# Optimization experiments

Hardware: AMD Instinct MI355X
Metric: run time of the kernel (lower is better)

The kernel has to match this reference:

```python
import jax, jax.numpy as jnp
import numpy as np

NUM_HEADS = 4
OUTPUT_DIM = 64


def setup_inputs() -> dict:
    key = jax.random.key(0)
    k1, k2, k3 = jax.random.split(key, 3)
    B, N, F = 8, 2048, 256
    features = jax.random.normal(k1, (B, N, F), dtype=jnp.float32)
    adj_matrix = jax.random.uniform(k2, (B, N, N), dtype=jnp.float32)
    # learned params (glorot-ish scale)
    kernel = jax.random.normal(k3, (F, OUTPUT_DIM * NUM_HEADS), dtype=jnp.float32) * (1.0 / np.sqrt(F))
    bias = jnp.zeros((OUTPUT_DIM * NUM_HEADS,), dtype=jnp.float32)
    return {"features": features, "adj_matrix": adj_matrix, "kernel": kernel, "bias": bias}


def reference(features, adj_matrix, kernel, bias):
    B, N, F = features.shape
    H, D = NUM_HEADS, OUTPUT_DIM
    Wh = jnp.matmul(features, kernel)                 # [B, N, H*D]
    Whh = Wh.reshape(B, N, H, D)                      # [B, N, H, D]
    # per-node, per-head score: inner product Wh1 @ Wh2 = ||Wh||^2
    e = jnp.sum(Whh * Whh, axis=-1)                   # [B, N, H]
    attention = jax.nn.softmax(e, axis=1)             # softmax over nodes
    attention = jnp.mean(attention, axis=2)           # head mean -> [B, N]
    # adjacency mask (broadcast column score over neighbors)
    A = attention[:, :, None] * adj_matrix            # [B, N, N]
    out = jnp.matmul(A, Wh) + bias                    # [B, N, H*D]
    return jax.nn.relu(out)
```

## Files before the change

### kernel.cpp

```cpp
#include <hip/hip_runtime.h>
#include <hip/hip_bf16.h>

#define BATCH 8
#define NNODE 2048
#define FDIM 256
#define HD 256
#define NH 4
#define MROWS (BATCH*NNODE)

typedef float f32x4 __attribute__((ext_vector_type(4)));
typedef short s16x8 __attribute__((ext_vector_type(8)));
typedef unsigned short ushort_t;

#define MFMA __builtin_amdgcn_mfma_f32_16x16x32_bf16
#define SCHED0() __builtin_amdgcn_sched_barrier(0)
#define SBAR() __builtin_amdgcn_s_barrier()

__device__ __forceinline__ void split2(float f, ushort_t& h, ushort_t& l) {
    unsigned u = __builtin_bit_cast(unsigned, f);
    h = (ushort_t)(u >> 16);
    float fh = __builtin_bit_cast(float, u & 0xffff0000u);
    float lo = f - fh;
    l = (ushort_t)(__builtin_bit_cast(unsigned, lo) >> 16);
}

#define GLOAD16(gp, lp) __builtin_amdgcn_global_load_lds( \
    (const __attribute__((address_space(1))) void*)(gp),  \
    (__attribute__((address_space(3))) void*)(lp), 16, 0, 0)

__global__ __launch_bounds__(256) void wprep_kernel(
    const float* __restrict__ Wm,
    ushort_t* __restrict__ wt_hi, ushort_t* __restrict__ wt_lo)
{
    const int nn = blockIdx.x, k = threadIdx.x;
    ushort_t h, l;
    split2(Wm[(size_t)k * HD + nn], h, l);
    wt_hi[nn * FDIM + k] = h;
    wt_lo[nn * FDIM + k] = l;
}

__global__ __launch_bounds__(256, 4) void gemm1_kernel(
    const float* __restrict__ features,
    const ushort_t* __restrict__ wt_hi,
    const ushort_t* __restrict__ wt_lo,
    ushort_t* __restrict__ WhT_hi,
    ushort_t* __restrict__ WhT_lo,
    float* __restrict__ e_out)
{
    __shared__ __align__(16) ushort_t Ah[64 * 64];
    __shared__ __align__(16) ushort_t Al[64 * 64];
    __shared__ __align__(16) ushort_t Bh[64 * 64];
    __shared__ __align__(16) ushort_t Bl[64 * 64];
    __shared__ float red[64][2];

    const int tid = threadIdx.x, lane = tid & 63, w = tid >> 6;
    const int wr = w >> 1, wc = w & 1;
    const int row0 = blockIdx.x * 64;
    const int head = blockIdx.y;
    const int col0 = head * 64;

    const float* Ab = features + (size_t)row0 * FDIM;
    const ushort_t* Bhg = wt_hi + (size_t)col0 * FDIM;
    const ushort_t* Blg = wt_lo + (size_t)col0 * FDIM;

    const int sr0 = tid >> 3;
    const int sg8 = tid & 7;
    const int bc = (lane >> 3);
    const int bs = lane & 7;

    f32x4 ar[4];
    f32x4 acc[2][2];
    #pragma unroll
    for (int m = 0; m < 2; ++m)
        #pragma unroll
        for (int n = 0; n < 2; ++n) acc[m][n] = (f32x4)0.f;

    #define G1_LOADA(K0) do {                                                  \
        _Pragma("unroll")                                                      \
        for (int i = 0; i < 2; ++i) {                                          \
            const int r = sr0 + 32 * i;                                        \
            ar[2*i]   = *(const f32x4*)&Ab[(size_t)r * FDIM + (K0) + sg8 * 8]; \
            ar[2*i+1] = *(const f32x4*)&Ab[(size_t)r * FDIM + (K0) + sg8 * 8 + 4]; \
        }                                                                      \
    } while (0)

    #define G1_STAGEA() do {                                                   \
        _Pragma("unroll")                                                      \
        for (int i = 0; i < 2; ++i) {                                          \
            const int r = sr0 + 32 * i;                                        \
            s16x8 vh, vl; ushort_t hh, ll;                                     \
            _Pragma("unroll")                                                  \
            for (int j = 0; j < 4; ++j) {                                      \
                split2(ar[2*i][j], hh, ll);  vh[j] = (short)hh; vl[j] = (short)ll; \
            }                                                                  \
            _Pragma("unroll")                                                  \
            for (int j = 0; j < 4; ++j) {                                      \
                split2(ar[2*i+1][j], hh, ll); vh[4+j] = (short)hh; vl[4+j] = (short)ll; \
            }                                                                  \
            const int off = r * 64 + ((sg8 ^ (r & 7)) << 3);                   \
            *(s16x8*)&Ah[off] = vh; *(s16x8*)&Al[off] = vl;                    \
        }                                                                      \
    } while (0)

    #define G1_STAGEB(K0) do {                                                 \
        _Pragma("unroll")                                                      \
        for (int qq = 0; qq < 2; ++qq) {                                       \
            const int q = w + qq * 4;                                          \
            const int c = q * 8 + bc;                                          \
            const int g = bs ^ (c & 7);                                        \
            GLOAD16(&Bhg[(size_t)c * FDIM + (K0) + g * 8], &Bh[q * 512]);      \
            GLOAD16(&Blg[(size_t)c * FDIM + (K0) + g * 8], &Bl[q * 512]);      \
        }                                                                      \
    } while (0)

    G1_LOADA(0);
    for (int t = 0; t < 4; ++t) {
        G1_STAGEB(t * 64);
        G1_STAGEA();
        if (t < 3) G1_LOADA((t + 1) * 64);
        if (t < 3) { asm volatile("s_waitcnt lgkmcnt(0) vmcnt(4)" ::: "memory"); }
        else       { asm volatile("s_waitcnt lgkmcnt(0) vmcnt(0)" ::: "memory"); }
        SCHED0(); SBAR(); SCHED0();
        #pragma unroll
        for (int kh = 0; kh < 2; ++kh) {
            const int kg = kh * 4 + (lane >> 4);
            s16x8 afh[2], afl[2], bfh[2], bfl[2];
            #pragma unroll
            for (int m = 0; m < 2; ++m) {
                const int r = wr * 32 + m * 16 + (lane & 15);
                const int off = r * 64 + ((kg ^ (r & 7)) << 3);
                afh[m] = *(const s16x8*)&Ah[off];
                afl[m] = *(const s16x8*)&Al[off];
            }
            #pragma unroll
            for (int n = 0; n < 2; ++n) {
                const int c = wc * 32 + n * 16 + (lane & 15);
                const int off = c * 64 + ((kg ^ (c & 7)) << 3);
                bfh[n] = *(const s16x8*)&Bh[off];
                bfl[n] = *(const s16x8*)&Bl[off];
            }
            #pragma unroll
            for (int m = 0; m < 2; ++m)
                #pragma unroll
                for (int n = 0; n < 2; ++n) {
                    acc[m][n] = MFMA(afh[m], bfh[n], acc[m][n], 0, 0, 0);
                    acc[m][n] = MFMA(afh[m], bfl[n], acc[m][n], 0, 0, 0);
                    acc[m][n] = MFMA(afl[m], bfh[n], acc[m][n], 0, 0, 0);
                }
        }
        SCHED0(); SBAR(); SCHED0();
    }

    #pragma unroll
    for (int m = 0; m < 2; ++m)
        #pragma unroll
        for (int j = 0; j < 4; ++j) {
            float p = acc[m][0][j] * acc[m][0][j] + acc[m][1][j] * acc[m][1][j];
            p += __shfl_xor(p, 1, 64);
            p += __shfl_xor(p, 2, 64);
            p += __shfl_xor(p, 4, 64);
            p += __shfl_xor(p, 8, 64);
            if ((lane & 15) == 0)
                red[wr * 32 + m * 16 + (lane >> 4) * 4 + j][wc] = p;
        }

    __syncthreads();
    ushort_t* Th = Ah;
    ushort_t* Tl = Al;
    #pragma unroll
    for (int m = 0; m < 2; ++m)
        #pragma unroll
        for (int n = 0; n < 2; ++n)
            #pragma unroll
            for (int j = 0; j < 4; ++j) {
                const int rr = wr * 32 + m * 16 + (lane >> 4) * 4 + j;
                const int cc = wc * 32 + n * 16 + (lane & 15);
                const int ad = cc * 64 + ((((rr >> 3) ^ (cc & 7))) << 3) + (rr & 7);
                ushort_t hh, ll;
                split2(acc[m][n][j], hh, ll);
                Th[ad] = hh; Tl[ad] = ll;
            }
    __syncthreads();

    if (tid < 64) {
        const int rg = row0 + tid;
        e_out[((size_t)((rg >> 11) * NH + head)) * NNODE + (rg & 2047)] =
            red[tid][0] + red[tid][1];
    }
    const int bb = row0 >> 11, node0 = row0 & 2047;
    #pragma unroll
    for (int i = 0; i < 2; ++i) {
        const int gid = tid + 256 * i;
        const int c = gid >> 3, gr = gid & 7;
        const int ad = c * 64 + ((gr ^ (c & 7)) << 3);
        uint4 vh = *(const uint4*)&Th[ad];
        uint4 vl = *(const uint4*)&Tl[ad];
        const size_t o = ((size_t)bb * HD + col0 + c) * NNODE + node0 + gr * 8;
        *(uint4*)&WhT_hi[o] = vh;
        *(uint4*)&WhT_lo[o] = vl;
    }
}

__global__ __launch_bounds__(256) void sm_kernel(
    const float* __restrict__ e, float* __restrict__ ms)
{
    __shared__ float red[8];
    const int bh = blockIdx.x, tid = threadIdx.x;
    const int lane = tid & 63, w = tid >> 6;
    const float* row = e + (size_t)bh * NNODE;
    float mx = -3.0e38f;
    for (int n = tid; n < NNODE; n += 256) mx = fmaxf(mx, row[n]);
    #pragma unroll
    for (int off = 32; off; off >>= 1) mx = fmaxf(mx, __shfl_xor(mx, off, 64));
    if (lane == 0) red[w] = mx;
    __syncthreads();
    mx = fmaxf(fmaxf(red[0], red[1]), fmaxf(red[2], red[3]));
    float s = 0.f;
    for (int n = tid; n < NNODE; n += 256) s += expf(row[n] - mx);
    #pragma unroll
    for (int off = 32; off; off >>= 1) s += __shfl_xor(s, off, 64);
    if (lane == 0) red[4 + w] = s;
    __syncthreads();
    if (tid == 0) {
        ms[bh * 2] = mx;
        ms[bh * 2 + 1] = red[4] + red[5] + red[6] + red[7];
    }
}

__global__ __launch_bounds__(256) void att_kernel(
    const float* __restrict__ e, const float* __restrict__ ms,
    float* __restrict__ attv)
{
    const int i = blockIdx.x * 256 + threadIdx.x;
    const int b = i >> 11, n = i & 2047;
    float a = 0.f;
    #pragma unroll
    for (int h = 0; h < NH; ++h) {
        const int bh = b * NH + h;
        a += expf(e[(size_t)bh * NNODE + n] - ms[bh * 2]) / ms[bh * 2 + 1];
    }
    attv[i] = 0.25f * a;
}

__global__ __launch_bounds__(256, 2) void gemm2_kernel(
    const float* __restrict__ adj,
    const ushort_t* __restrict__ WhT_hi,
    const ushort_t* __restrict__ WhT_lo,
    const float* __restrict__ att,
    const float* __restrict__ bias,
    float* __restrict__ out)
{
    __shared__ __align__(16) ushort_t Bh[3][64 * 64];
    __shared__ __align__(16) ushort_t Bl[3][64 * 64];

    const int tid = threadIdx.x, lane = tid & 63, w = tid >> 6;
    const int b = blockIdx.z;
    const int row0 = blockIdx.x * 128, col0 = blockIdx.y * 64;

    const ushort_t* Bhg = WhT_hi + ((size_t)b * HD + col0) * NNODE;
    const ushort_t* Blg = WhT_lo + ((size_t)b * HD + col0) * NNODE;

    const float* pA = adj + (size_t)b * NNODE * NNODE
                    + (size_t)(row0 + w * 32 + (lane & 15)) * NNODE
                    + ((lane >> 4) * 8);

    const int bc = lane >> 3, bs = lane & 7;

    f32x4 ar[2][2][2];
    s16x8 afh[2][2], afl[2][2];
    f32x4 acc[2][4];
    #pragma unroll
    for (int m = 0; m < 2; ++m)
        #pragma unroll
        for (int n = 0; n < 4; ++n) acc[m][n] = (f32x4)0.f;

    #define G2_LOADA(K0) do {                                                   \
        _Pragma("unroll")                                                       \
        for (int m = 0; m < 2; ++m)                                             \
        _Pragma("unroll")                                                       \
        for (int ks = 0; ks < 2; ++ks) {                                        \
            ar[m][ks][0] = *(const f32x4*)&pA[(size_t)m * 16 * NNODE + (K0) + ks * 32]; \
            ar[m][ks][1] = *(const f32x4*)&pA[(size_t)m * 16 * NNODE + (K0) + ks * 32 + 4]; \
        }                                                                       \
    } while (0)

    #define G2_CONVERT() do {                                                   \
        _Pragma("unroll")                                                       \
        for (int m = 0; m < 2; ++m)                                             \
        _Pragma("unroll")                                                       \
        for (int ks = 0; ks < 2; ++ks) {                                        \
            ushort_t hh, ll;                                                    \
            _Pragma("unroll")                                                   \
            for (int h2 = 0; h2 < 2; ++h2)                                      \
            _Pragma("unroll")                                                   \
            for (int j = 0; j < 4; ++j) {                                       \
                split2(ar[m][ks][h2][j], hh, ll);                               \
                afh[m][ks][h2 * 4 + j] = (short)hh;                             \
                afl[m][ks][h2 * 4 + j] = (short)ll;                             \
            }                                                                   \
        }                                                                       \
    } while (0)

    #define G2_STAGEB(BUF, K0) do {                                             \
        _Pragma("unroll")                                                       \
        for (int qq = 0; qq < 2; ++qq) {                                        \
            const int q = w + qq * 4;                                           \
            const int c = q * 8 + bc;                                           \
            const int g = bs ^ (c & 7);                                         \
            GLOAD16(&Bhg[(size_t)c * NNODE + (K0) + g * 8], &Bh[BUF][q * 512]); \
            GLOAD16(&Blg[(size_t)c * NNODE + (K0) + g * 8], &Bl[BUF][q * 512]); \
        }                                                                       \
    } while (0)

    #define G2_COMPUTE(BHP, BLP) do {                                           \
        _Pragma("unroll")                                                       \
        for (int ks = 0; ks < 2; ++ks) {                                        \
            const int kg = ks * 4 + (lane >> 4);                                \
            s16x8 bfh[4], bfl[4];                                               \
            _Pragma("unroll")                                                   \
            for (int n = 0; n < 4; ++n) {                                       \
                const int c = n * 16 + (lane & 15);                             \
                const int off = c * 64 + ((kg ^ (c & 7)) << 3);                 \
                bfh[n] = *(const s16x8*)&(BHP)[off];                            \
                bfl[n] = *(const s16x8*)&(BLP)[off];                            \
            }                                                                   \
            __builtin_amdgcn_s_setprio(1);                                      \
            _Pragma("unroll")                                                   \
            for (int m = 0; m < 2; ++m)                                         \
            _Pragma("unroll")                                                   \
            for (int n = 0; n < 4; ++n) {                                       \
                acc[m][n] = MFMA(afh[m][ks], bfh[n], acc[m][n], 0, 0, 0);       \
                acc[m][n] = MFMA(afh[m][ks], bfl[n], acc[m][n], 0, 0, 0);       \
                acc[m][n] = MFMA(afl[m][ks], bfh[n], acc[m][n], 0, 0, 0);       \
            }                                                                   \
            __builtin_amdgcn_s_setprio(0);                                      \
        }                                                                       \
    } while (0)

    G2_STAGEB(0, 0);
    G2_LOADA(0);

    int cur = 0;
    for (int t = 0; t < 32; ++t) {
        const int nxt = (cur == 2) ? 0 : cur + 1;
        if (t < 31) G2_STAGEB(nxt, (t + 1) * 64);
        G2_CONVERT();
        if (t < 31) G2_LOADA((t + 1) * 64);
        asm volatile("s_waitcnt vmcnt(12)" ::: "memory");
        SCHED0(); SBAR(); SCHED0();
        {
            const ushort_t* bhp = &Bh[cur][0];
            const ushort_t* blp = &Bl[cur][0];
            G2_COMPUTE(bhp, blp);
        }
        cur = nxt;
    }

    const float* attb = att + (size_t)b * NNODE;
    #pragma unroll
    for (int n = 0; n < 4; ++n) {
        const int c = col0 + n * 16 + (lane & 15);
        const float bv = bias[c];
        #pragma unroll
        for (int m = 0; m < 2; ++m)
            #pragma unroll
            for (int j = 0; j < 4; ++j) {
                const int row = row0 + w * 32 + m * 16 + (lane >> 4) * 4 + j;
                out[((size_t)b * NNODE + row) * HD + c] =
                    fmaxf(fmaf(acc[m][n][j], attb[row], bv), 0.f);
            }
    }
}

extern "C" void kernel_launch(void* const* d_in, const int* in_sizes, int n_in,
                              void* d_out, int out_size, void* d_ws, size_t ws_size,
                              hipStream_t stream) {
    const float* features = (const float*)d_in[0];
    const float* adj      = (const float*)d_in[1];
    const float* Wm       = (const float*)d_in[2];
    const float* bias     = (const float*)d_in[3];
    float* out = (float*)d_out;

    ushort_t* WhT_hi = (ushort_t*)d_ws;
    ushort_t* WhT_lo = WhT_hi + (size_t)BATCH * HD * NNODE;
    ushort_t* wt_hi  = WhT_lo + (size_t)BATCH * HD * NNODE;
    ushort_t* wt_lo  = wt_hi + FDIM * HD;
    float* e    = (float*)(wt_lo + FDIM * HD);
    float* ms   = e + (size_t)BATCH * NH * NNODE;
    float* attv = ms + 64;

    wprep_kernel<<<HD, 256, 0, stream>>>(Wm, wt_hi, wt_lo);
    gemm1_kernel<<<dim3(MROWS / 64, NH), 256, 0, stream>>>(
        features, wt_hi, wt_lo, WhT_hi, WhT_lo, e);
    sm_kernel<<<BATCH * NH, 256, 0, stream>>>(e, ms);
    att_kernel<<<MROWS / 256, 256, 0, stream>>>(e, ms, attv);
    gemm2_kernel<<<dim3(NNODE / 128, HD / 64, BATCH), 256, 0, stream>>>(
        adj, WhT_hi, WhT_lo, attv, bias, out);
}
```

Before: 276.8 us.

## Load B fragments directly from global into registers, dropping LDS staging

The second GEMM no longer stages the bf16 hi/lo WhT tiles through a triple-buffered LDS ring with barriers. Each lane now loads its B fragments straight from global memory into registers, using a manual two-stage register double buffer for A and B-hi, and loads B-lo just in time. This removes LDS traffic and block-wide barriers, but each wave now reads B redundantly from global/L2 and register pressure rises (the occupancy hint of 2 was dropped). It also relies on the compiler's waitcnt placement instead of explicit ones.

Result: slower. 353.2 us (+27.6%).

```diff
diff --git a/kernel.cpp b/kernel.cpp
--- a/kernel.cpp
+++ b/kernel.cpp
@@ -242,7 +242,7 @@
     attv[i] = 0.25f * a;
 }
 
-__global__ __launch_bounds__(256, 2) void gemm2_kernel(
+__global__ __launch_bounds__(256) void gemm2_kernel(
     const float* __restrict__ adj,
     const ushort_t* __restrict__ WhT_hi,
     const ushort_t* __restrict__ WhT_lo,
@@ -250,23 +250,19 @@
     const float* __restrict__ bias,
     float* __restrict__ out)
 {
-    __shared__ __align__(16) ushort_t Bh[3][64 * 64];
-    __shared__ __align__(16) ushort_t Bl[3][64 * 64];
-
     const int tid = threadIdx.x, lane = tid & 63, w = tid >> 6;
     const int b = blockIdx.z;
     const int row0 = blockIdx.x * 128, col0 = blockIdx.y * 64;
 
-    const ushort_t* Bhg = WhT_hi + ((size_t)b * HD + col0) * NNODE;
-    const ushort_t* Blg = WhT_lo + ((size_t)b * HD + col0) * NNODE;
-
     const float* pA = adj + (size_t)b * NNODE * NNODE
                     + (size_t)(row0 + w * 32 + (lane & 15)) * NNODE
                     + ((lane >> 4) * 8);
-
-    const int bc = lane >> 3, bs = lane & 7;
-
-    f32x4 ar[2][2][2];
+    const size_t bbase = ((size_t)b * HD + col0 + (lane & 15)) * NNODE + ((lane >> 4) * 8);
+    const ushort_t* pBh = WhT_hi + bbase;
+    const ushort_t* pBl = WhT_lo + bbase;
+
+    f32x4 a0[8], a1[8];
+    s16x8 bh0[8], bh1[8], bl_[8];
     s16x8 afh[2][2], afl[2][2];
     f32x4 acc[2][4];
     #pragma unroll
@@ -274,17 +270,33 @@
         #pragma unroll
         for (int n = 0; n < 4; ++n) acc[m][n] = (f32x4)0.f;
 
-    #define G2_LOADA(K0) do {                                                   \
+    #define G2_LOADA(AR, K0) do {                                               \
         _Pragma("unroll")                                                       \
         for (int m = 0; m < 2; ++m)                                             \
         _Pragma("unroll")                                                       \
         for (int ks = 0; ks < 2; ++ks) {                                        \
-            ar[m][ks][0] = *(const f32x4*)&pA[(size_t)m * 16 * NNODE + (K0) + ks * 32]; \
-            ar[m][ks][1] = *(const f32x4*)&pA[(size_t)m * 16 * NNODE + (K0) + ks * 32 + 4]; \
+            AR[m*4 + ks*2 + 0] = *(const f32x4*)&pA[(size_t)m * 16 * NNODE + (K0) + ks * 32]; \
+            AR[m*4 + ks*2 + 1] = *(const f32x4*)&pA[(size_t)m * 16 * NNODE + (K0) + ks * 32 + 4]; \
         }                                                                       \
     } while (0)
 
-    #define G2_CONVERT() do {                                                   \
+    #define G2_LOADBH(BH, K0) do {                                              \
+        _Pragma("unroll")                                                       \
+        for (int n = 0; n < 4; ++n)                                             \
+        _Pragma("unroll")                                                       \
+        for (int ks = 0; ks < 2; ++ks)                                          \
+            BH[n*2 + ks] = *(const s16x8*)&pBh[(size_t)n * 16 * NNODE + (K0) + ks * 32]; \
+    } while (0)
+
+    #define G2_LOADBL(BL, K0) do {                                              \
+        _Pragma("unroll")                                                       \
+        for (int n = 0; n < 4; ++n)                                             \
+        _Pragma("unroll")                                                       \
+        for (int ks = 0; ks < 2; ++ks)                                          \
+            BL[n*2 + ks] = *(const s16x8*)&pBl[(size_t)n * 16 * NNODE + (K0) + ks * 32]; \
+    } while (0)
+
+    #define G2_CONVERT(AR) do {                                                 \
         _Pragma("unroll")                                                       \
         for (int m = 0; m < 2; ++m)                                             \
         _Pragma("unroll")                                                       \
@@ -294,66 +306,46 @@
             for (int h2 = 0; h2 < 2; ++h2)                                      \
             _Pragma("unroll")                                                   \
             for (int j = 0; j < 4; ++j) {                                       \
-                split2(ar[m][ks][h2][j], hh, ll);                               \
+                split2(AR[m*4 + ks*2 + h2][j], hh, ll);                         \
                 afh[m][ks][h2 * 4 + j] = (short)hh;                             \
                 afl[m][ks][h2 * 4 + j] = (short)ll;                             \
             }                                                                   \
         }                                                                       \
     } while (0)
 
-    #define G2_STAGEB(BUF, K0) do {                                             \
-        _Pragma("unroll")                                                       \
-        for (int qq = 0; qq < 2; ++qq) {                                        \
-            const int q = w + qq * 4;                                           \
-            const int c = q * 8 + bc;                                           \
-            const int g = bs ^ (c & 7);                                         \
-            GLOAD16(&Bhg[(size_t)c * NNODE + (K0) + g * 8], &Bh[BUF][q * 512]); \
-            GLOAD16(&Blg[(size_t)c * NNODE + (K0) + g * 8], &Bl[BUF][q * 512]); \
-        }                                                                       \
-    } while (0)
-
-    #define G2_COMPUTE(BHP, BLP) do {                                           \
+    #define G2_MFMA(BH, BL) do {                                                \
         _Pragma("unroll")                                                       \
         for (int ks = 0; ks < 2; ++ks) {                                        \
-            const int kg = ks * 4 + (lane >> 4);                                \
-            s16x8 bfh[4], bfl[4];                                               \
-            _Pragma("unroll")                                                   \
-            for (int n = 0; n < 4; ++n) {                                       \
-                const int c = n * 16 + (lane & 15);                             \
-                const int off = c * 64 + ((kg ^ (c & 7)) << 3);                 \
-                bfh[n] = *(const s16x8*)&(BHP)[off];                            \
-                bfl[n] = *(const s16x8*)&(BLP)[off];                            \
-            }                                                                   \
             __builtin_amdgcn_s_setprio(1);                                      \
             _Pragma("unroll")                                                   \
             for (int m = 0; m < 2; ++m)                                         \
             _Pragma("unroll")                                                   \
             for (int n = 0; n < 4; ++n) {                                       \
-                acc[m][n] = MFMA(afh[m][ks], bfh[n], acc[m][n], 0, 0, 0);       \
-                acc[m][n] = MFMA(afh[m][ks], bfl[n], acc[m][n], 0, 0, 0);       \
-                acc[m][n] = MFMA(afl[m][ks], bfh[n], acc[m][n], 0, 0, 0);       \
+                acc[m][n] = MFMA(afh[m][ks], BH[n*2+ks], acc[m][n], 0, 0, 0);   \
+                acc[m][n] = MFMA(afh[m][ks], BL[n*2+ks], acc[m][n], 0, 0, 0);   \
+                acc[m][n] = MFMA(afl[m][ks], BH[n*2+ks], acc[m][n], 0, 0, 0);   \
             }                                                                   \
             __builtin_amdgcn_s_setprio(0);                                      \
         }                                                                       \
     } while (0)
 
-    G2_STAGEB(0, 0);
-    G2_LOADA(0);
-
-    int cur = 0;
-    for (int t = 0; t < 32; ++t) {
-        const int nxt = (cur == 2) ? 0 : cur + 1;
-        if (t < 31) G2_STAGEB(nxt, (t + 1) * 64);
-        G2_CONVERT();
-        if (t < 31) G2_LOADA((t + 1) * 64);
-        asm volatile("s_waitcnt vmcnt(12)" ::: "memory");
-        SCHED0(); SBAR(); SCHED0();
-        {
-            const ushort_t* bhp = &Bh[cur][0];
-            const ushort_t* blp = &Bl[cur][0];
-            G2_COMPUTE(bhp, blp);
+    G2_LOADBH(bh0, 0);
+    G2_LOADA(a0, 0);
+
+    #pragma unroll 1
+    for (int t = 0; t < 32; t += 2) {
+        G2_LOADBL(bl_, t * 64);
+        G2_LOADBH(bh1, (t + 1) * 64);
+        G2_LOADA(a1, (t + 1) * 64);
+        G2_CONVERT(a0);
+        G2_MFMA(bh0, bl_);
+        G2_LOADBL(bl_, (t + 1) * 64);
+        if (t + 2 < 32) {
+            G2_LOADBH(bh0, (t + 2) * 64);
+            G2_LOADA(a0, (t + 2) * 64);
         }
-        cur = nxt;
+        G2_CONVERT(a1);
+        G2_MFMA(bh1, bl_);
     }
 
     const float* attb = att + (size_t)b * NNODE;
```

## Drop adjacency low-part split in gemm2 and remap blocks for XCD locality

Applied to the files above, without the earlier changes.

The adjacency operand is now rounded to a single bf16 value instead of a hi/lo pair, which removes one of the three MFMAs per tile and the lo-part conversion. The Wh operand keeps its hi/lo split, and the two remaining MFMA groups are reordered into separate loops. The 3D grid becomes a 1D grid of 512 blocks, remapped so that consecutive block IDs on the same XCD share the same batch and B columns, which should improve L2 reuse. The cost is lower precision on the adjacency values, with a risk of accuracy drift in the output.

Measured after the change: 267.7 us. 3.3% less time.

```diff
diff --git a/kernel.cpp b/kernel.cpp
--- a/kernel.cpp
+++ b/kernel.cpp
@@ -16,6 +16,11 @@
 #define SCHED0() __builtin_amdgcn_sched_barrier(0)
 #define SBAR() __builtin_amdgcn_s_barrier()
 
+__device__ __forceinline__ ushort_t f2bf(float f) {
+    unsigned u = __builtin_bit_cast(unsigned, f);
+    u += 0x7fffu + ((u >> 16) & 1u);
+    return (ushort_t)(u >> 16);
+}
 __device__ __forceinline__ void split2(float f, ushort_t& h, ushort_t& l) {
     unsigned u = __builtin_bit_cast(unsigned, f);
     h = (ushort_t)(u >> 16);
@@ -254,8 +259,11 @@
     __shared__ __align__(16) ushort_t Bl[3][64 * 64];
 
     const int tid = threadIdx.x, lane = tid & 63, w = tid >> 6;
-    const int b = blockIdx.z;
-    const int row0 = blockIdx.x * 128, col0 = blockIdx.y * 64;
+
+    const int bid = blockIdx.x;
+    const int wg = (bid & 7) * 64 + (bid >> 3);
+    const int bx = wg & 15, by = (wg >> 4) & 3, b = wg >> 6;
+    const int row0 = bx * 128, col0 = by * 64;
 
     const ushort_t* Bhg = WhT_hi + ((size_t)b * HD + col0) * NNODE;
     const ushort_t* Blg = WhT_lo + ((size_t)b * HD + col0) * NNODE;
@@ -267,7 +275,7 @@
     const int bc = lane >> 3, bs = lane & 7;
 
     f32x4 ar[2][2][2];
-    s16x8 afh[2][2], afl[2][2];
+    s16x8 afh[2][2];
     f32x4 acc[2][4];
     #pragma unroll
     for (int m = 0; m < 2; ++m)
@@ -288,17 +296,12 @@
         _Pragma("unroll")                                                       \
         for (int m = 0; m < 2; ++m)                                             \
         _Pragma("unroll")                                                       \
-        for (int ks = 0; ks < 2; ++ks) {                                        \
-            ushort_t hh, ll;                                                    \
-            _Pragma("unroll")                                                   \
-            for (int h2 = 0; h2 < 2; ++h2)                                      \
-            _Pragma("unroll")                                                   \
-            for (int j = 0; j < 4; ++j) {                                       \
-                split2(ar[m][ks][h2][j], hh, ll);                               \
-                afh[m][ks][h2 * 4 + j] = (short)hh;                             \
-                afl[m][ks][h2 * 4 + j] = (short)ll;                             \
-            }                                                                   \
-        }                                                                       \
+        for (int ks = 0; ks < 2; ++ks)                                          \
+        _Pragma("unroll")                                                       \
+        for (int h2 = 0; h2 < 2; ++h2)                                          \
+        _Pragma("unroll")                                                       \
+        for (int j = 0; j < 4; ++j)                                             \
+            afh[m][ks][h2 * 4 + j] = (short)f2bf(ar[m][ks][h2][j]);             \
     } while (0)
 
     #define G2_STAGEB(BUF, K0) do {                                             \
@@ -328,11 +331,13 @@
             _Pragma("unroll")                                                   \
             for (int m = 0; m < 2; ++m)                                         \
             _Pragma("unroll")                                                   \
-            for (int n = 0; n < 4; ++n) {                                       \
+            for (int n = 0; n < 4; ++n)                                         \
                 acc[m][n] = MFMA(afh[m][ks], bfh[n], acc[m][n], 0, 0, 0);       \
+            _Pragma("unroll")                                                   \
+            for (int m = 0; m < 2; ++m)                                         \
+            _Pragma("unroll")                                                   \
+            for (int n = 0; n < 4; ++n)                                         \
                 acc[m][n] = MFMA(afh[m][ks], bfl[n], acc[m][n], 0, 0, 0);       \
-                acc[m][n] = MFMA(afl[m][ks], bfh[n], acc[m][n], 0, 0, 0);       \
-            }                                                                   \
             __builtin_amdgcn_s_setprio(0);                                      \
         }                                                                       \
     } while (0)
@@ -394,6 +399,6 @@
         features, wt_hi, wt_lo, WhT_hi, WhT_lo, e);
     sm_kernel<<<BATCH * NH, 256, 0, stream>>>(e, ms);
     att_kernel<<<MROWS / 256, 256, 0, stream>>>(e, ms, attv);
-    gemm2_kernel<<<dim3(NNODE / 128, HD / 64, BATCH), 256, 0, stream>>>(
+    gemm2_kernel<<<512, 256, 0, stream>>>(
         adj, WhT_hi, WhT_lo, attv, bias, out);
 }
```
